# Kernel optimization log

Hardware: AMD Instinct MI355X
Metric: run time of the kernel (lower is better)

## Reference

```python
import jax, jax.numpy as jnp
import numpy as np

N = 50000   # nodes
E = 800000  # edges
H = 128     # hidden dim
V = 50000   # feats_per_node (embedding vocab)


def setup_inputs() -> dict:
    key = jax.random.key(0)
    ks = jax.random.split(key, 16)
    s = 0.05  # keep activations in a sane range
    return {
        "node_ids": jax.random.randint(ks[0], (N,), 0, V),
        "src": jax.random.randint(ks[1], (E,), 0, N),
        "dst": jnp.sort(jax.random.randint(ks[2], (E,), 0, N)),
        "emb": jax.random.normal(ks[3], (V, H), jnp.float32) * s,
        "W_pool1": jax.random.normal(ks[4], (H, H), jnp.float32) * s,
        "b_pool1": jax.random.normal(ks[5], (H,), jnp.float32) * s,
        "W_self1": jax.random.normal(ks[6], (H, H), jnp.float32) * s,
        "W_neigh1": jax.random.normal(ks[7], (H, H), jnp.float32) * s,
        "b1": jax.random.normal(ks[8], (H,), jnp.float32) * s,
        "W_pool2": jax.random.normal(ks[9], (H, H), jnp.float32) * s,
        "b_pool2": jax.random.normal(ks[10], (H,), jnp.float32) * s,
        "W_self2": jax.random.normal(ks[11], (H, H), jnp.float32) * s,
        "W_neigh2": jax.random.normal(ks[12], (H, H), jnp.float32) * s,
        "b2": jax.random.normal(ks[13], (H,), jnp.float32) * s,
    }


def _sage_pool_layer(h, src, dst, W_pool, b_pool, W_self, W_neigh, b):
    # DGL SAGEConv('pool'): per-src MLP, gather over edges, segmented max per dst.
    m = jax.nn.relu(h @ W_pool + b_pool)              # [N, H]
    msgs = m[src]                                     # [E, H] gather
    agg = jax.ops.segment_max(msgs, dst, num_segments=N,
                              indices_are_sorted=True)  # [N, H]
    agg = jnp.where(jnp.isneginf(agg), 0.0, agg)      # zero-in-degree -> 0 (DGL semantics)
    return h @ W_self + agg @ W_neigh + b


def reference(node_ids, src, dst, emb,
              W_pool1, b_pool1, W_self1, W_neigh1, b1,
              W_pool2, b_pool2, W_self2, W_neigh2, b2):
    h = emb[node_ids]                                 # embedding_h on 1-hot indices
    h = _sage_pool_layer(h, src, dst, W_pool1, b_pool1, W_self1, W_neigh1, b1)
    h = _sage_pool_layer(h, src, dst, W_pool2, b_pool2, W_self2, W_neigh2, b2)
    return h
```

## Files before the change

### kernel.cpp

```cpp
#include <hip/hip_runtime.h>

#define HD 128

typedef __attribute__((ext_vector_type(8))) short short8;
typedef __attribute__((ext_vector_type(4))) float floatx4;
typedef __attribute__((ext_vector_type(2))) unsigned short ushort2v;
typedef __attribute__((ext_vector_type(4))) unsigned int uint4v;

typedef unsigned short ushort_t;
typedef unsigned int uint_t;

__device__ __forceinline__ ushort_t f2b(float f) {
    union { float f; uint_t u; } v; v.f = f;
    uint_t r = v.u + 0x7fff + ((v.u >> 16) & 1);
    return (ushort_t)(r >> 16);
}
__device__ __forceinline__ short8 cvt8(const float* __restrict__ p) {
    float4 u = *(const float4*)p, v = *(const float4*)(p + 4);
    short8 r;
    r[0] = (short)f2b(u.x); r[1] = (short)f2b(u.y); r[2] = (short)f2b(u.z); r[3] = (short)f2b(u.w);
    r[4] = (short)f2b(v.x); r[5] = (short)f2b(v.y); r[6] = (short)f2b(v.z); r[7] = (short)f2b(v.w);
    return r;
}
__device__ __forceinline__ uint_t pkmax(uint_t a, uint_t b) {
    return __builtin_bit_cast(uint_t,
        __builtin_elementwise_max(__builtin_bit_cast(ushort2v, a),
                                  __builtin_bit_cast(ushort2v, b)));
}

__global__ __launch_bounds__(256) void k_prep(const int* __restrict__ dst, int E,
                                              int* __restrict__ rp, int N,
                                              const float* W0, const float* W1,
                                              const float* W2, const float* W3,
                                              const float* W4, const float* W5,
                                              ushort_t* __restrict__ Wpk, int nbR) {
    int b = blockIdx.x;
    if (b < nbR) {
        int i = b * 256 + threadIdx.x;
        if (i > N) return;
        int lo = 0, hi = E;
        while (lo < hi) {
            int mid = (lo + hi) >> 1;
            if (dst[mid] < i) lo = mid + 1; else hi = mid;
        }
        rp[i] = lo;
    } else {
        int bb = b - nbR;
        const float* Ws[6] = {W0, W1, W2, W3, W4, W5};
        int mat = bb >> 6;
        int o = ((bb & 63) << 8) + threadIdx.x;
        int j = o & 7, l = (o >> 3) & 63, s = (o >> 9) & 3, t = o >> 11;
        int k = s * 32 + ((l >> 4) & 3) * 8 + j;
        int n = t * 16 + (l & 15);
        Wpk[(size_t)mat * 16384 + o] = f2b(Ws[mat][k * HD + n]);
    }
}

__device__ __forceinline__ void stage_w(const ushort_t* __restrict__ g,
                                        ushort_t* l, int tid) {
#pragma unroll
    for (int i = 0; i < 8; ++i) {
        int off = i * 2048 + tid * 8;
        *(short8*)&l[off] = *(const short8*)&g[off];
    }
}

__device__ __forceinline__ void store_bf16(ushort_t* __restrict__ m, int row,
                                           int colbase, const floatx4& acc,
                                           const float4& bv, bool relu, int N) {
    if (row >= N) return;
    float v0 = acc[0] + bv.x, v1 = acc[1] + bv.y, v2 = acc[2] + bv.z, v3 = acc[3] + bv.w;
    if (relu) { v0 = fmaxf(v0, 0.f); v1 = fmaxf(v1, 0.f); v2 = fmaxf(v2, 0.f); v3 = fmaxf(v3, 0.f); }
    uint2 o; o.x = (uint_t)f2b(v0) | ((uint_t)f2b(v1) << 16);
    o.y = (uint_t)f2b(v2) | ((uint_t)f2b(v3) << 16);
    *(uint2*)&m[(size_t)row * HD + colbase] = o;
}

__device__ __forceinline__ void store_m(ushort_t* __restrict__ m, int row,
                                        int colbase, const floatx4& acc,
                                        const float4& bv, int N) {
    if (row >= N) return;
    float v0 = fmaxf(acc[0] + bv.x, 0.f), v1 = fmaxf(acc[1] + bv.y, 0.f);
    float v2 = fmaxf(acc[2] + bv.z, 0.f), v3 = fmaxf(acc[3] + bv.w, 0.f);
    uint2 o; o.x = (uint_t)f2b(v0) | ((uint_t)f2b(v1) << 16);
    o.y = (uint_t)f2b(v2) | ((uint_t)f2b(v3) << 16);
    size_t addr = (size_t)(colbase >> 5) * ((size_t)N * 32)
                + (size_t)row * 32 + (colbase & 31);
    *(uint2*)&m[addr] = o;
}

__global__ __launch_bounds__(256) void k_gather_pool(const int* __restrict__ ids,
                                                     const float* __restrict__ emb,
                                                     const ushort_t* __restrict__ Wpk,
                                                     const float* __restrict__ bias,
                                                     ushort_t* __restrict__ h0,
                                                     ushort_t* __restrict__ m, int N) {
    __shared__ ushort_t Wl[16384];
    int wave = blockIdx.x * 4 + (threadIdx.x >> 6);
    int row0 = wave * 32;
    int l = threadIdx.x & 63;
    int ar0 = row0 + (l & 15); if (ar0 >= N) ar0 = N - 1;
    int ar1 = ar0 + 16;        if (ar1 >= N) ar1 = N - 1;
    int ac = (l >> 4) * 8;
    int id0 = ids[ar0], id1 = ids[ar1];
    short8 a0[4], a1[4];
#pragma unroll
    for (int s = 0; s < 4; ++s) {
        a0[s] = cvt8(&emb[(size_t)id0 * HD + s * 32 + ac]);
        a1[s] = cvt8(&emb[(size_t)id1 * HD + s * 32 + ac]);
    }
    stage_w(Wpk, Wl, threadIdx.x);
    __syncthreads();
    if (row0 >= N) return;
#pragma unroll
    for (int s = 0; s < 4; ++s) {
        *(short8*)&h0[(size_t)ar0 * HD + s * 32 + ac] = a0[s];
        *(short8*)&h0[(size_t)ar1 * HD + s * 32 + ac] = a1[s];
    }
    int g0 = row0 + (l & 15), g1 = g0 + 16;
    int cb0 = ((l >> 4) & 3) * 4;
#pragma unroll
    for (int t = 0; t < 8; ++t) {
        floatx4 acc0 = {0.f, 0.f, 0.f, 0.f};
        floatx4 acc1 = {0.f, 0.f, 0.f, 0.f};
#pragma unroll
        for (int s = 0; s < 4; ++s) {
            short8 w = *(const short8*)&Wl[(t * 4 + s) * 512 + l * 8];
            acc0 = __builtin_amdgcn_mfma_f32_16x16x32_bf16(w, a0[s], acc0, 0, 0, 0);
            acc1 = __builtin_amdgcn_mfma_f32_16x16x32_bf16(w, a1[s], acc1, 0, 0, 0);
        }
        int cb = t * 16 + cb0;
        float4 bv = *(const float4*)&bias[cb];
        store_m(m, g0, cb, acc0, bv, N);
        store_m(m, g1, cb, acc1, bv, N);
    }
}

__global__ __launch_bounds__(256) void k_pool(const ushort_t* __restrict__ h,
                                              const ushort_t* __restrict__ Wpk,
                                              const float* __restrict__ bias,
                                              ushort_t* __restrict__ m, int N) {
    __shared__ ushort_t Wl[16384];
    int wave = blockIdx.x * 4 + (threadIdx.x >> 6);
    int row0 = wave * 32;
    int l = threadIdx.x & 63;
    int ar0 = row0 + (l & 15); if (ar0 >= N) ar0 = N - 1;
    int ar1 = ar0 + 16;        if (ar1 >= N) ar1 = N - 1;
    int ac = (l >> 4) * 8;
    short8 a0[4], a1[4];
#pragma unroll
    for (int s = 0; s < 4; ++s) {
        a0[s] = *(const short8*)&h[(size_t)ar0 * HD + s * 32 + ac];
        a1[s] = *(const short8*)&h[(size_t)ar1 * HD + s * 32 + ac];
    }
    stage_w(Wpk, Wl, threadIdx.x);
    __syncthreads();
    if (row0 >= N) return;
    int g0 = row0 + (l & 15), g1 = g0 + 16;
    int cb0 = ((l >> 4) & 3) * 4;
#pragma unroll
    for (int t = 0; t < 8; ++t) {
        floatx4 acc0 = {0.f, 0.f, 0.f, 0.f};
        floatx4 acc1 = {0.f, 0.f, 0.f, 0.f};
#pragma unroll
        for (int s = 0; s < 4; ++s) {
            short8 w = *(const short8*)&Wl[(t * 4 + s) * 512 + l * 8];
            acc0 = __builtin_amdgcn_mfma_f32_16x16x32_bf16(w, a0[s], acc0, 0, 0, 0);
            acc1 = __builtin_amdgcn_mfma_f32_16x16x32_bf16(w, a1[s], acc1, 0, 0, 0);
        }
        int cb = t * 16 + cb0;
        float4 bv = *(const float4*)&bias[cb];
        store_m(m, g0, cb, acc0, bv, N);
        store_m(m, g1, cb, acc1, bv, N);
    }
}

__global__ __launch_bounds__(256) void k_segmax(const ushort_t* __restrict__ m,
                                                const int* __restrict__ src,
                                                const int* __restrict__ rp,
                                                ushort_t* __restrict__ agg, int N) {
    int cg = blockIdx.x & 3;
    int l = threadIdx.x & 63;
    int slot = l >> 2;
    int c = l & 3;
    int node0 = ((blockIdx.x >> 2) * 4 + (threadIdx.x >> 6)) * 4;
    if (node0 >= N) return;
    const uint_t* __restrict__ mg = (const uint_t*)m + (size_t)cg * ((size_t)N * 16);
    uint_t* __restrict__ aggw = (uint_t*)agg;

    int bg[4], en[4], sv[4], deg[4];
#pragma unroll
    for (int nn = 0; nn < 4; ++nn) {
        int node = node0 + nn;
        bg[nn] = (node < N) ? rp[node] : 0;
        en[nn] = (node < N) ? rp[node + 1] : 0;
        deg[nn] = en[nn] - bg[nn];
    }
#pragma unroll
    for (int nn = 0; nn < 4; ++nn) {
        int si = bg[nn] + l, lim = en[nn] - 1;
        si = si > lim ? lim : si; si = si < 0 ? 0 : si;
        sv[nn] = __builtin_nontemporal_load(&src[si]);
    }

    uint4v p0[4], p1[4];
#pragma unroll
    for (int nn = 0; nn < 4; ++nn) {
        if (deg[nn] > 0) {
            int i0 = slot; if (i0 > deg[nn] - 1) i0 = deg[nn] - 1;
            int s0 = __shfl(sv[nn], i0);
            p0[nn] = *(const uint4v*)&mg[(size_t)s0 * 16 + c * 4];
        }
        if (deg[nn] > 16) {
            int i1 = 16 + slot; if (i1 > deg[nn] - 1) i1 = deg[nn] - 1;
            int s1 = __shfl(sv[nn], i1);
            p1[nn] = *(const uint4v*)&mg[(size_t)s1 * 16 + c * 4];
        }
    }

    int b0 = slot & 1, b1 = (slot >> 1) & 1;
#pragma unroll
    for (int nn = 0; nn < 4; ++nn) {
        int node = node0 + nn;
        if (node >= N) continue;
        uint_t a0 = 0u, a1 = 0u, a2 = 0u, a3 = 0u;
        if (deg[nn] > 0) { a0 = p0[nn].x; a1 = p0[nn].y; a2 = p0[nn].z; a3 = p0[nn].w; }
        if (deg[nn] > 16) {
            a0 = pkmax(a0, p1[nn].x); a1 = pkmax(a1, p1[nn].y);
            a2 = pkmax(a2, p1[nn].z); a3 = pkmax(a3, p1[nn].w);
        }
        if (deg[nn] > 32) {
            int beg = bg[nn], end = en[nn];
            int svc = sv[nn];
            int last = (end - beg < 64 ? end - beg : 64) - 1;
            for (int o = 32; o <= last; o += 16) {
                int i = o + slot; if (i > last) i = last;
                int s = __shfl(svc, i);
                uint4v p = *(const uint4v*)&mg[(size_t)s * 16 + c * 4];
                a0 = pkmax(a0, p.x); a1 = pkmax(a1, p.y);
                a2 = pkmax(a2, p.z); a3 = pkmax(a3, p.w);
            }
            for (int base = beg + 64; base < end; base += 64) {
                int lim = end - 1;
                int si = base + l; if (si > lim) si = lim;
                svc = __builtin_nontemporal_load(&src[si]);
                int nb = end - base; if (nb > 64) nb = 64;
                int lst = nb - 1;
                for (int o = 0; o <= lst; o += 16) {
                    int i = o + slot; if (i > lst) i = lst;
                    int s = __shfl(svc, i);
                    uint4v p = *(const uint4v*)&mg[(size_t)s * 16 + c * 4];
                    a0 = pkmax(a0, p.x); a1 = pkmax(a1, p.y);
                    a2 = pkmax(a2, p.z); a3 = pkmax(a3, p.w);
                }
            }
        }
        uint_t q0 = b0 ? a2 : a0, q1 = b0 ? a3 : a1;
        uint_t r0 = b0 ? a0 : a2, r1 = b0 ? a1 : a3;
        q0 = pkmax(q0, (uint_t)__shfl_xor((int)r0, 4));
        q1 = pkmax(q1, (uint_t)__shfl_xor((int)r1, 4));
        uint_t s_ = b1 ? q1 : q0, t_ = b1 ? q0 : q1;
        s_ = pkmax(s_, (uint_t)__shfl_xor((int)t_, 8));
        s_ = pkmax(s_, (uint_t)__shfl_xor((int)s_, 16));
        s_ = pkmax(s_, (uint_t)__shfl_xor((int)s_, 32));
        if (slot < 4)
            __builtin_nontemporal_store(s_,
                &aggw[(size_t)node * 64 + cg * 16 + c * 4 + 2 * b0 + b1]);
    }
}

template <bool F32OUT>
__global__ __launch_bounds__(256) void k_dual(const ushort_t* __restrict__ h,
                                              const ushort_t* __restrict__ agg,
                                              const ushort_t* __restrict__ WsPk,
                                              const ushort_t* __restrict__ WnPk,
                                              const float* __restrict__ bias,
                                              void* __restrict__ outp, int N) {
    __shared__ ushort_t Wl[32768];
    int wave = blockIdx.x * 4 + (threadIdx.x >> 6);
    int row0 = wave * 32;
    int l = threadIdx.x & 63;
    int ar0 = row0 + (l & 15); if (ar0 >= N) ar0 = N - 1;
    int ar1 = ar0 + 16;        if (ar1 >= N) ar1 = N - 1;
    int ac = (l >> 4) * 8;
    short8 ah0[4], ah1[4], ag0[4], ag1[4];
#pragma unroll
    for (int s = 0; s < 4; ++s) {
        ah0[s] = *(const short8*)&h[(size_t)ar0 * HD + s * 32 + ac];
        ah1[s] = *(const short8*)&h[(size_t)ar1 * HD + s * 32 + ac];
        ag0[s] = *(const short8*)&agg[(size_t)ar0 * HD + s * 32 + ac];
        ag1[s] = *(const short8*)&agg[(size_t)ar1 * HD + s * 32 + ac];
    }
    stage_w(WsPk, Wl, threadIdx.x);
    stage_w(WnPk, Wl + 16384, threadIdx.x);
    __syncthreads();
    if (row0 >= N) return;
    int g0 = row0 + (l & 15), g1 = g0 + 16;
    int cb0 = ((l >> 4) & 3) * 4;
#pragma unroll
    for (int t = 0; t < 8; ++t) {
        floatx4 acc0 = {0.f, 0.f, 0.f, 0.f};
        floatx4 acc1 = {0.f, 0.f, 0.f, 0.f};
#pragma unroll
        for (int s = 0; s < 4; ++s) {
            short8 ws = *(const short8*)&Wl[(t * 4 + s) * 512 + l * 8];
            acc0 = __builtin_amdgcn_mfma_f32_16x16x32_bf16(ws, ah0[s], acc0, 0, 0, 0);
            acc1 = __builtin_amdgcn_mfma_f32_16x16x32_bf16(ws, ah1[s], acc1, 0, 0, 0);
        }
#pragma unroll
        for (int s = 0; s < 4; ++s) {
            short8 wn = *(const short8*)&Wl[16384 + (t * 4 + s) * 512 + l * 8];
            acc0 = __builtin_amdgcn_mfma_f32_16x16x32_bf16(wn, ag0[s], acc0, 0, 0, 0);
            acc1 = __builtin_amdgcn_mfma_f32_16x16x32_bf16(wn, ag1[s], acc1, 0, 0, 0);
        }
        int cb = t * 16 + cb0;
        float4 bv = *(const float4*)&bias[cb];
        if (F32OUT) {
            float* out = (float*)outp;
            if (g0 < N) {
                float4 v = make_float4(acc0[0] + bv.x, acc0[1] + bv.y,
                                       acc0[2] + bv.z, acc0[3] + bv.w);
                *(float4*)&out[(size_t)g0 * HD + cb] = v;
            }
            if (g1 < N) {
                float4 v = make_float4(acc1[0] + bv.x, acc1[1] + bv.y,
                                       acc1[2] + bv.z, acc1[3] + bv.w);
                *(float4*)&out[(size_t)g1 * HD + cb] = v;
            }
        } else {
            ushort_t* out = (ushort_t*)outp;
            store_bf16(out, g0, cb, acc0, bv, false, N);
            store_bf16(out, g1, cb, acc1, bv, false, N);
        }
    }
}

extern "C" void kernel_launch(void* const* d_in, const int* in_sizes, int n_in,
                              void* d_out, int out_size, void* d_ws, size_t ws_size,
                              hipStream_t stream) {
    const int*   node_ids = (const int*)d_in[0];
    const int*   src      = (const int*)d_in[1];
    const int*   dst      = (const int*)d_in[2];
    const float* emb      = (const float*)d_in[3];
    const float* Wp1      = (const float*)d_in[4];
    const float* bp1      = (const float*)d_in[5];
    const float* Ws1      = (const float*)d_in[6];
    const float* Wn1      = (const float*)d_in[7];
    const float* b1       = (const float*)d_in[8];
    const float* Wp2      = (const float*)d_in[9];
    const float* bp2      = (const float*)d_in[10];
    const float* Ws2      = (const float*)d_in[11];
    const float* Wn2      = (const float*)d_in[12];
    const float* b2       = (const float*)d_in[13];
    float* out = (float*)d_out;

    const int N = in_sizes[0];
    const int E = in_sizes[1];

    char* ws = (char*)d_ws;
    int* rp = (int*)ws;
    size_t off = (((size_t)(N + 1) * 4) + 255) & ~(size_t)255;
    ushort_t* Wpk  = (ushort_t*)(ws + off);
    ushort_t* h0   = Wpk + 6 * 16384;
    ushort_t* h1   = h0 + (size_t)N * HD;
    ushort_t* bufM = h1 + (size_t)N * HD;
    ushort_t* bufA = bufM + (size_t)N * HD;

    const int nbR = (N + 1 + 255) / 256;
    const int nbP = 6 * 64;
    const int nb_gemm = (N + 127) / 128;
    const int nb_seg  = ((N + 15) / 16) * 4;

    k_prep<<<nbR + nbP, 256, 0, stream>>>(dst, E, rp, N,
                                          Wp1, Ws1, Wn1, Wp2, Ws2, Wn2, Wpk, nbR);

    const ushort_t* Wp1k = Wpk;
    const ushort_t* Ws1k = Wpk + 16384;
    const ushort_t* Wn1k = Wpk + 2 * 16384;
    const ushort_t* Wp2k = Wpk + 3 * 16384;
    const ushort_t* Ws2k = Wpk + 4 * 16384;
    const ushort_t* Wn2k = Wpk + 5 * 16384;

    k_gather_pool<<<nb_gemm, 256, 0, stream>>>(node_ids, emb, Wp1k, bp1, h0, bufM, N);
    k_segmax<<<nb_seg, 256, 0, stream>>>(bufM, src, rp, bufA, N);
    k_dual<false><<<nb_gemm, 256, 0, stream>>>(h0, bufA, Ws1k, Wn1k, b1, h1, N);
    k_pool<<<nb_gemm, 256, 0, stream>>>(h1, Wp2k, bp2, bufM, N);
    k_segmax<<<nb_seg, 256, 0, stream>>>(bufM, src, rp, bufA, N);
    k_dual<true><<<nb_gemm, 256, 0, stream>>>(h1, bufA, Ws2k, Wn2k, b2, out, N);
}
```

Measured before the change: 246.7 us.

## Precompute padded per-node source lists and split GEMM kernels by column half

Adds a prep stage that builds a fixed 32-slot padded source-index table per node, so segmax reads neighbor indices directly instead of doing clamped loads and shuffles. Nodes with more than 32 edges fall back to direct src reads. The pool and dual GEMM kernels are also split into two column halves, which halves shared memory per block and doubles the grid to raise occupancy. The cost is re-reading the A operand twice, an extra 6.4MB index table with its own prep work, and extra binary searches in prep.

```diff
diff --git a/kernel.cpp b/kernel.cpp
--- a/kernel.cpp
+++ b/kernel.cpp
@@ -27,24 +27,30 @@
         __builtin_elementwise_max(__builtin_bit_cast(ushort2v, a),
                                   __builtin_bit_cast(ushort2v, b)));
 }
+__device__ __forceinline__ int lbound(const int* __restrict__ dst, int E, int v) {
+    int lo = 0, hi = E;
+    while (lo < hi) {
+        int mid = (lo + hi) >> 1;
+        if (dst[mid] < v) lo = mid + 1; else hi = mid;
+    }
+    return lo;
+}
 
 __global__ __launch_bounds__(256) void k_prep(const int* __restrict__ dst, int E,
+                                              const int* __restrict__ src,
                                               int* __restrict__ rp, int N,
+                                              int* __restrict__ srcPad,
                                               const float* W0, const float* W1,
                                               const float* W2, const float* W3,
                                               const float* W4, const float* W5,
-                                              ushort_t* __restrict__ Wpk, int nbR) {
+                                              ushort_t* __restrict__ Wpk,
+                                              int nbR, int nbP) {
     int b = blockIdx.x;
     if (b < nbR) {
         int i = b * 256 + threadIdx.x;
         if (i > N) return;
-        int lo = 0, hi = E;
-        while (lo < hi) {
-            int mid = (lo + hi) >> 1;
-            if (dst[mid] < i) lo = mid + 1; else hi = mid;
-        }
-        rp[i] = lo;
-    } else {
+        rp[i] = lbound(dst, E, i);
+    } else if (b < nbR + nbP) {
         int bb = b - nbR;
         const float* Ws[6] = {W0, W1, W2, W3, W4, W5};
         int mat = bb >> 6;
@@ -53,6 +59,21 @@
         int k = s * 32 + ((l >> 4) & 3) * 8 + j;
         int n = t * 16 + (l & 15);
         Wpk[(size_t)mat * 16384 + o] = f2b(Ws[mat][k * HD + n]);
+    } else {
+        int idx = (b - nbR - nbP) * 256 + threadIdx.x;
+        int node = idx >> 5;
+        if (node >= N) return;
+        int j = idx & 31;
+        int lane = threadIdx.x & 63;
+        int half = (lane & 31) >> 4;
+        int lo = lbound(dst, E, node + half);
+        int base = lane & 32;
+        int beg = __shfl(lo, base);
+        int end = __shfl(lo, base + 16);
+        int deg = end - beg;
+        int val = 0;
+        if (deg > 0) val = src[beg + (j < deg ? j : deg - 1)];
+        srcPad[(size_t)node * 32 + j] = val;
     }
 }
 
@@ -60,6 +81,14 @@
                                         ushort_t* l, int tid) {
 #pragma unroll
     for (int i = 0; i < 8; ++i) {
+        int off = i * 2048 + tid * 8;
+        *(short8*)&l[off] = *(const short8*)&g[off];
+    }
+}
+__device__ __forceinline__ void stage_w_half(const ushort_t* __restrict__ g,
+                                             ushort_t* l, int tid) {
+#pragma unroll
+    for (int i = 0; i < 4; ++i) {
         int off = i * 2048 + tid * 8;
         *(short8*)&l[off] = *(const short8*)&g[off];
     }
@@ -140,8 +169,9 @@
                                               const ushort_t* __restrict__ Wpk,
                                               const float* __restrict__ bias,
                                               ushort_t* __restrict__ m, int N) {
-    __shared__ ushort_t Wl[16384];
-    int wave = blockIdx.x * 4 + (threadIdx.x >> 6);
+    __shared__ ushort_t Wl[8192];
+    int colhalf = blockIdx.x & 1;
+    int wave = (blockIdx.x >> 1) * 4 + (threadIdx.x >> 6);
     int row0 = wave * 32;
     int l = threadIdx.x & 63;
     int ar0 = row0 + (l & 15); if (ar0 >= N) ar0 = N - 1;
@@ -153,13 +183,13 @@
         a0[s] = *(const short8*)&h[(size_t)ar0 * HD + s * 32 + ac];
         a1[s] = *(const short8*)&h[(size_t)ar1 * HD + s * 32 + ac];
     }
-    stage_w(Wpk, Wl, threadIdx.x);
+    stage_w_half(Wpk + colhalf * 8192, Wl, threadIdx.x);
     __syncthreads();
     if (row0 >= N) return;
     int g0 = row0 + (l & 15), g1 = g0 + 16;
     int cb0 = ((l >> 4) & 3) * 4;
 #pragma unroll
-    for (int t = 0; t < 8; ++t) {
+    for (int t = 0; t < 4; ++t) {
         floatx4 acc0 = {0.f, 0.f, 0.f, 0.f};
         floatx4 acc1 = {0.f, 0.f, 0.f, 0.f};
 #pragma unroll
@@ -168,7 +198,7 @@
             acc0 = __builtin_amdgcn_mfma_f32_16x16x32_bf16(w, a0[s], acc0, 0, 0, 0);
             acc1 = __builtin_amdgcn_mfma_f32_16x16x32_bf16(w, a1[s], acc1, 0, 0, 0);
         }
-        int cb = t * 16 + cb0;
+        int cb = (colhalf * 4 + t) * 16 + cb0;
         float4 bv = *(const float4*)&bias[cb];
         store_m(m, g0, cb, acc0, bv, N);
         store_m(m, g1, cb, acc1, bv, N);
@@ -176,6 +206,7 @@
 }
 
 __global__ __launch_bounds__(256) void k_segmax(const ushort_t* __restrict__ m,
+                                                const int* __restrict__ srcPad,
                                                 const int* __restrict__ src,
                                                 const int* __restrict__ rp,
                                                 ushort_t* __restrict__ agg, int N) {
@@ -188,71 +219,47 @@
     const uint_t* __restrict__ mg = (const uint_t*)m + (size_t)cg * ((size_t)N * 16);
     uint_t* __restrict__ aggw = (uint_t*)agg;
 
-    int bg[4], en[4], sv[4], deg[4];
+    int nd[4], s0[4], s1[4], deg[4];
 #pragma unroll
     for (int nn = 0; nn < 4; ++nn) {
-        int node = node0 + nn;
-        bg[nn] = (node < N) ? rp[node] : 0;
-        en[nn] = (node < N) ? rp[node + 1] : 0;
-        deg[nn] = en[nn] - bg[nn];
+        int node = node0 + nn; if (node >= N) node = N - 1;
+        nd[nn] = node;
     }
 #pragma unroll
     for (int nn = 0; nn < 4; ++nn) {
-        int si = bg[nn] + l, lim = en[nn] - 1;
-        si = si > lim ? lim : si; si = si < 0 ? 0 : si;
-        sv[nn] = __builtin_nontemporal_load(&src[si]);
-    }
-
+        s0[nn] = srcPad[(size_t)nd[nn] * 32 + slot];
+        s1[nn] = srcPad[(size_t)nd[nn] * 32 + 16 + slot];
+    }
+#pragma unroll
+    for (int nn = 0; nn < 4; ++nn)
+        deg[nn] = rp[nd[nn] + 1] - rp[nd[nn]];
     uint4v p0[4], p1[4];
 #pragma unroll
     for (int nn = 0; nn < 4; ++nn) {
-        if (deg[nn] > 0) {
-            int i0 = slot; if (i0 > deg[nn] - 1) i0 = deg[nn] - 1;
-            int s0 = __shfl(sv[nn], i0);
-            p0[nn] = *(const uint4v*)&mg[(size_t)s0 * 16 + c * 4];
-        }
-        if (deg[nn] > 16) {
-            int i1 = 16 + slot; if (i1 > deg[nn] - 1) i1 = deg[nn] - 1;
-            int s1 = __shfl(sv[nn], i1);
-            p1[nn] = *(const uint4v*)&mg[(size_t)s1 * 16 + c * 4];
-        }
-    }
-
+        p0[nn] = *(const uint4v*)&mg[(size_t)s0[nn] * 16 + c * 4];
+        p1[nn] = *(const uint4v*)&mg[(size_t)s1[nn] * 16 + c * 4];
+    }
     int b0 = slot & 1, b1 = (slot >> 1) & 1;
 #pragma unroll
     for (int nn = 0; nn < 4; ++nn) {
         int node = node0 + nn;
         if (node >= N) continue;
         uint_t a0 = 0u, a1 = 0u, a2 = 0u, a3 = 0u;
-        if (deg[nn] > 0) { a0 = p0[nn].x; a1 = p0[nn].y; a2 = p0[nn].z; a3 = p0[nn].w; }
-        if (deg[nn] > 16) {
-            a0 = pkmax(a0, p1[nn].x); a1 = pkmax(a1, p1[nn].y);
-            a2 = pkmax(a2, p1[nn].z); a3 = pkmax(a3, p1[nn].w);
+        if (deg[nn] > 0) {
+            a0 = pkmax(p0[nn].x, p1[nn].x);
+            a1 = pkmax(p0[nn].y, p1[nn].y);
+            a2 = pkmax(p0[nn].z, p1[nn].z);
+            a3 = pkmax(p0[nn].w, p1[nn].w);
         }
         if (deg[nn] > 32) {
-            int beg = bg[nn], end = en[nn];
-            int svc = sv[nn];
-            int last = (end - beg < 64 ? end - beg : 64) - 1;
-            for (int o = 32; o <= last; o += 16) {
-                int i = o + slot; if (i > last) i = last;
-                int s = __shfl(svc, i);
+            int beg = rp[node];
+            int dm1 = deg[nn] - 1;
+            for (int o = 32; o < deg[nn]; o += 16) {
+                int i = o + slot; if (i > dm1) i = dm1;
+                int s = src[beg + i];
                 uint4v p = *(const uint4v*)&mg[(size_t)s * 16 + c * 4];
                 a0 = pkmax(a0, p.x); a1 = pkmax(a1, p.y);
                 a2 = pkmax(a2, p.z); a3 = pkmax(a3, p.w);
-            }
-            for (int base = beg + 64; base < end; base += 64) {
-                int lim = end - 1;
-                int si = base + l; if (si > lim) si = lim;
-                svc = __builtin_nontemporal_load(&src[si]);
-                int nb = end - base; if (nb > 64) nb = 64;
-                int lst = nb - 1;
-                for (int o = 0; o <= lst; o += 16) {
-                    int i = o + slot; if (i > lst) i = lst;
-                    int s = __shfl(svc, i);
-                    uint4v p = *(const uint4v*)&mg[(size_t)s * 16 + c * 4];
-                    a0 = pkmax(a0, p.x); a1 = pkmax(a1, p.y);
-                    a2 = pkmax(a2, p.z); a3 = pkmax(a3, p.w);
-                }
             }
         }
         uint_t q0 = b0 ? a2 : a0, q1 = b0 ? a3 : a1;
@@ -276,8 +283,9 @@
                                               const ushort_t* __restrict__ WnPk,
                                               const float* __restrict__ bias,
                                               void* __restrict__ outp, int N) {
-    __shared__ ushort_t Wl[32768];
-    int wave = blockIdx.x * 4 + (threadIdx.x >> 6);
+    __shared__ ushort_t Wl[16384];
+    int colhalf = blockIdx.x & 1;
+    int wave = (blockIdx.x >> 1) * 4 + (threadIdx.x >> 6);
     int row0 = wave * 32;
     int l = threadIdx.x & 63;
     int ar0 = row0 + (l & 15); if (ar0 >= N) ar0 = N - 1;
@@ -291,14 +299,14 @@
         ag0[s] = *(const short8*)&agg[(size_t)ar0 * HD + s * 32 + ac];
         ag1[s] = *(const short8*)&agg[(size_t)ar1 * HD + s * 32 + ac];
     }
-    stage_w(WsPk, Wl, threadIdx.x);
-    stage_w(WnPk, Wl + 16384, threadIdx.x);
+    stage_w_half(WsPk + colhalf * 8192, Wl, threadIdx.x);
+    stage_w_half(WnPk + colhalf * 8192, Wl + 8192, threadIdx.x);
     __syncthreads();
     if (row0 >= N) return;
     int g0 = row0 + (l & 15), g1 = g0 + 16;
     int cb0 = ((l >> 4) & 3) * 4;
 #pragma unroll
-    for (int t = 0; t < 8; ++t) {
+    for (int t = 0; t < 4; ++t) {
         floatx4 acc0 = {0.f, 0.f, 0.f, 0.f};
         floatx4 acc1 = {0.f, 0.f, 0.f, 0.f};
 #pragma unroll
@@ -309,11 +317,11 @@
         }
 #pragma unroll
         for (int s = 0; s < 4; ++s) {
-            short8 wn = *(const short8*)&Wl[16384 + (t * 4 + s) * 512 + l * 8];
+            short8 wn = *(const short8*)&Wl[8192 + (t * 4 + s) * 512 + l * 8];
             acc0 = __builtin_amdgcn_mfma_f32_16x16x32_bf16(wn, ag0[s], acc0, 0, 0, 0);
             acc1 = __builtin_amdgcn_mfma_f32_16x16x32_bf16(wn, ag1[s], acc1, 0, 0, 0);
         }
-        int cb = t * 16 + cb0;
+        int cb = (colhalf * 4 + t) * 16 + cb0;
         float4 bv = *(const float4*)&bias[cb];
         if (F32OUT) {
             float* out = (float*)outp;
@@ -360,6 +368,8 @@
     char* ws = (char*)d_ws;
     int* rp = (int*)ws;
     size_t off = (((size_t)(N + 1) * 4) + 255) & ~(size_t)255;
+    int* srcPad = (int*)(ws + off);
+    off += (((size_t)N * 32 * 4) + 255) & ~(size_t)255;
     ushort_t* Wpk  = (ushort_t*)(ws + off);
     ushort_t* h0   = Wpk + 6 * 16384;
     ushort_t* h1   = h0 + (size_t)N * HD;
@@ -368,11 +378,14 @@
 
     const int nbR = (N + 1 + 255) / 256;
     const int nbP = 6 * 64;
+    const int nbS = ((N * 32) + 255) / 256;
     const int nb_gemm = (N + 127) / 128;
+    const int nb_half = nb_gemm * 2;
     const int nb_seg  = ((N + 15) / 16) * 4;
 
-    k_prep<<<nbR + nbP, 256, 0, stream>>>(dst, E, rp, N,
-                                          Wp1, Ws1, Wn1, Wp2, Ws2, Wn2, Wpk, nbR);
+    k_prep<<<nbR + nbP + nbS, 256, 0, stream>>>(dst, E, src, rp, N, srcPad,
+                                                Wp1, Ws1, Wn1, Wp2, Ws2, Wn2,
+                                                Wpk, nbR, nbP);
 
     const ushort_t* Wp1k = Wpk;
     const ushort_t* Ws1k = Wpk + 16384;
@@ -382,9 +395,9 @@
     const ushort_t* Wn2k = Wpk + 5 * 16384;
 
     k_gather_pool<<<nb_gemm, 256, 0, stream>>>(node_ids, emb, Wp1k, bp1, h0, bufM, N);
-    k_segmax<<<nb_seg, 256, 0, stream>>>(bufM, src, rp, bufA, N);
-    k_dual<false><<<nb_gemm, 256, 0, stream>>>(h0, bufA, Ws1k, Wn1k, b1, h1, N);
-    k_pool<<<nb_gemm, 256, 0, stream>>>(h1, Wp2k, bp2, bufM, N);
-    k_segmax<<<nb_seg, 256, 0, stream>>>(bufM, src, rp, bufA, N);
-    k_dual<true><<<nb_gemm, 256, 0, stream>>>(h1, bufA, Ws2k, Wn2k, b2, out, N);
-}
+    k_segmax<<<nb_seg, 256, 0, stream>>>(bufM, srcPad, src, rp, bufA, N);
+    k_dual<false><<<nb_half, 256, 0, stream>>>(h0, bufA, Ws1k, Wn1k, b1, h1, N);
+    k_pool<<<nb_half, 256, 0, stream>>>(h1, Wp2k, bp2, bufM, N);
+    k_segmax<<<nb_seg, 256, 0, stream>>>(bufM, srcPad, src, rp, bufA, N);
+    k_dual<true><<<nb_half, 256, 0, stream>>>(h1, bufA, Ws2k, Wn2k, b2, out, N);
+}
```

Measured after the change: 246.4 us. About the same (-0.1%).
